# Kernel optimization log

Measured on AMD Instinct MI355X. Metric: run time of the kernel, lower is better.

Reference implementation:

```python
import jax, jax.numpy as jnp
import numpy as np

K_TOP = 10  # module init k


def setup_inputs() -> dict:
    key = jax.random.key(0)
    k1, k2 = jax.random.split(key)
    B, C, H, W = 32, 512, 64, 64
    num_item = 100
    x = jax.random.normal(k1, (B, C, H, W), dtype=jnp.float32)
    # mempool initialized uniform(-stdv, stdv) with stdv = 1/sqrt(dim), as in init_memory
    stdv = 1.0 / np.sqrt(C)
    mempool = jax.random.uniform(k2, (num_item, C), minval=-stdv, maxval=stdv, dtype=jnp.float32)
    return {"x": x, "mempool": mempool}


def reference(x, mempool):
    B, C, H, W = x.shape
    # permute to channels-last, flatten spatial+batch -> queries [N, C]
    q = x.transpose(0, 2, 3, 1).reshape(-1, C)
    # attention over memory items: F.linear(query, mempool) == q @ mempool.T
    att = jax.nn.softmax(q @ mempool.T, axis=1)  # [N, num_item]
    val, idx = jax.lax.top_k(att, K_TOP)          # [N, k]
    val = jax.nn.softmax(val, axis=1)             # renormalize over top-k
    N = q.shape[0]
    # scatter renormalized weights back into a sparse attention matrix
    att_sp = jnp.zeros_like(att).at[jnp.arange(N)[:, None], idx].set(val)
    # reconstruct: F.linear(att, mempool.T) == att @ mempool
    out = (att_sp @ mempool).reshape(B, H, W, C).transpose(0, 3, 1, 2)
    # diversity loss on the memory pool
    m = mempool.shape[0]
    cosim = (mempool @ mempool.T) * 0.5
    off_diag = cosim * (1.0 - jnp.eye(m, dtype=cosim.dtype))
    loss = jnp.mean(jnp.abs(off_diag))
    return (out, loss)
```

## Files before the change

### kernel.cpp

```cpp
#include <hip/hip_runtime.h>
#include <math.h>

#define NITEM 100
#define CDIM 512
#define HW 4096
#define KTOP 10

typedef __attribute__((ext_vector_type(8))) short bf16x8;
typedef __attribute__((ext_vector_type(4))) float f32x4;

__device__ inline unsigned short bf16u(float f) {
  unsigned int u = __float_as_uint(f);
  u += 0x7fffu + ((u >> 16) & 1u);
  return (unsigned short)(u >> 16);
}

__global__ __launch_bounds__(256) __attribute__((amdgpu_waves_per_eu(3, 3)))
void logits_topk(
    const float* __restrict__ x, const float* __restrict__ mp,
    unsigned short* __restrict__ Wd)
{
  __shared__ float qs[2][32 * 128];
  __shared__ float ms[32 * 128];

  const int t   = threadIdx.x;
  const int tc  = t & 15;
  const int trg = t >> 4;
  const int n0  = blockIdx.x * 128;
  const int b   = n0 >> 12;
  const int sp0 = n0 & (HW - 1);
  const float* xb = x + (size_t)b * CDIM * HW + sp0;

  const int w = t >> 6, l = t & 63;
  const int item = t & 127;
  const int half = t >> 7;
  const float* mrow = mp + (size_t)(item < NITEM ? item : 0) * CDIM + 16 * half;

  auto issue_q = [&](int kt, int buf) {
    const int k0 = kt * 32;
    #pragma unroll
    for (int i = 0; i < 4; ++i) {
      const float* src = xb + (size_t)(k0 + 8 * w + 2 * i + (l >> 5)) * HW + (l & 31) * 4;
      float* dst = &qs[buf][(8 * w + 2 * i) * 128];
      __builtin_amdgcn_global_load_lds(
          (const __attribute__((address_space(1))) void*)src,
          (__attribute__((address_space(3))) void*)dst, 16, 0, 0);
    }
  };

  float acc[8][7];
  #pragma unroll
  for (int r = 0; r < 8; ++r)
    #pragma unroll
    for (int j = 0; j < 7; ++j) acc[r][j] = 0.f;

  issue_q(0, 0);
  float4 mv4[4];
  #pragma unroll
  for (int u = 0; u < 4; ++u) mv4[u] = *(const float4*)(mrow + 4 * u);

  int buf = 0;
  #pragma unroll 1
  for (int kt = 0; kt < 16; ++kt) {
    #pragma unroll
    for (int u = 0; u < 4; ++u) {
      ms[(16 * half + 4 * u + 0) * 128 + item] = mv4[u].x;
      ms[(16 * half + 4 * u + 1) * 128 + item] = mv4[u].y;
      ms[(16 * half + 4 * u + 2) * 128 + item] = mv4[u].z;
      ms[(16 * half + 4 * u + 3) * 128 + item] = mv4[u].w;
    }
    __syncthreads();
    if (kt < 15) {
      issue_q(kt + 1, buf ^ 1);
      const int k0n = (kt + 1) * 32;
      #pragma unroll
      for (int u = 0; u < 4; ++u) mv4[u] = *(const float4*)(mrow + k0n + 4 * u);
    }
    const float* qsb = qs[buf];
    #pragma unroll 2
    for (int kk = 0; kk < 32; ++kk) {
      const float* qr = qsb + kk * 128 + 8 * trg;
      const float* mr = ms + kk * 128 + tc;
      float4 qa = *(const float4*)(qr);
      float4 qb = *(const float4*)(qr + 4);
      float mm[7] = {mr[0], mr[16], mr[32], mr[48], mr[64], mr[80], mr[96]};
      float qq[8] = {qa.x, qa.y, qa.z, qa.w, qb.x, qb.y, qb.z, qb.w};
      #pragma unroll
      for (int r = 0; r < 8; ++r)
        #pragma unroll
        for (int j = 0; j < 7; ++j)
          acc[r][j] = __builtin_fmaf(qq[r], mm[j], acc[r][j]);
    }
    __syncthreads();
    buf ^= 1;
  }

  const int baserow = n0 + 8 * trg;
  #pragma unroll
  for (int r = 0; r < 8; ++r) {
    float attv[KTOP]; int id[KTOP];
    float mx = 0.f, Z = 0.f;
    #pragma unroll
    for (int s = 0; s < KTOP; ++s) {
      float bv = -INFINITY; int bi = 0x7fffffff;
      #pragma unroll
      for (int j = 0; j < 7; ++j) {
        bool valid = (j < 6) || (tc < 4);
        float v = valid ? acc[r][j] : -INFINITY;
        if (v > bv) { bv = v; bi = tc + 16 * j; }
      }
      #pragma unroll
      for (int d = 1; d < 16; d <<= 1) {
        float ov = __shfl_xor(bv, d, 16);
        int   oi = __shfl_xor(bi, d, 16);
        if (ov > bv || (ov == bv && oi < bi)) { bv = ov; bi = oi; }
      }
      if (s == 0) {
        mx = bv;
        float zp = 0.f;
        #pragma unroll
        for (int j = 0; j < 7; ++j) {
          bool valid = (j < 6) || (tc < 4);
          zp += valid ? __expf(acc[r][j] - mx) : 0.f;
        }
        #pragma unroll
        for (int d = 1; d < 16; d <<= 1) zp += __shfl_xor(zp, d, 16);
        Z = zp;
      }
      attv[s] = bv; id[s] = bi;
      #pragma unroll
      for (int j = 0; j < 7; ++j)
        if (bi == tc + 16 * j) acc[r][j] = -INFINITY;
    }
    float invZ = 1.f / Z;
    float p0 = invZ;
    float s2 = 0.f, wv[KTOP];
    #pragma unroll
    for (int s = 0; s < KTOP; ++s) {
      float p = __expf(attv[s] - mx) * invZ;
      float e = __expf(p - p0);
      wv[s] = e; s2 += e;
    }
    float inv2 = 1.f / s2;
    unsigned short wb[KTOP];
    #pragma unroll
    for (int s = 0; s < KTOP; ++s) wb[s] = bf16u(wv[s] * inv2);
    unsigned int packed[4];
    #pragma unroll
    for (int q2 = 0; q2 < 4; ++q2) {
      unsigned int lo = 0u, hi = 0u;
      #pragma unroll
      for (int s = 0; s < KTOP; ++s) {
        lo = (id[s] == 8 * tc + 2 * q2)     ? (unsigned int)wb[s] : lo;
        hi = (id[s] == 8 * tc + 2 * q2 + 1) ? (unsigned int)wb[s] : hi;
      }
      packed[q2] = lo | (hi << 16);
    }
    if (tc < 14) {
      uint4 o; o.x = packed[0]; o.y = packed[1]; o.z = packed[2]; o.w = packed[3];
      *(uint4*)(Wd + (size_t)(baserow + r) * 112 + 8 * tc) = o;
    }
  }
}

__global__ __launch_bounds__(256, 2) void recon(
    const float* __restrict__ mp, const unsigned short* __restrict__ Wd,
    float* __restrict__ out)
{
  __shared__ unsigned short Ash[128 * 136];
  __shared__ unsigned short Bsh[128 * 136];
  const int t  = threadIdx.x;
  const int ct = blockIdx.x & 3, nt = blockIdx.x >> 2;
  const int c0 = ct * 128, n0 = nt * 128;
  const int b  = n0 >> 12, sp0 = n0 & (HW - 1);

  #pragma unroll
  for (int j = 0; j < 13; ++j) {
    int task = t + 256 * j;
    if (task < 3200) {
      int k = task >> 5, c4 = (task & 31) << 2;
      float4 v = *(const float4*)(mp + (size_t)k * CDIM + c0 + c4);
      Ash[(c4 + 0) * 136 + k] = bf16u(v.x);
      Ash[(c4 + 1) * 136 + k] = bf16u(v.y);
      Ash[(c4 + 2) * 136 + k] = bf16u(v.z);
      Ash[(c4 + 3) * 136 + k] = bf16u(v.w);
    }
  }
  {
    int c = t >> 1, hf = t & 1;
    unsigned int* A32 = (unsigned int*)Ash;
    #pragma unroll
    for (int j = 0; j < 9; ++j) { int k = 100 + 2 * (hf * 9 + j); A32[(c * 136 + k) >> 1] = 0u; }
  }
  {
    int n = t >> 1, hf = t & 1;
    #pragma unroll
    for (int j = 0; j < 7; ++j) {
      int f = hf * 7 + j;
      *(bf16x8*)(Bsh + n * 136 + 8 * f) = *(const bf16x8*)(Wd + (size_t)(n0 + n) * 112 + 8 * f);
    }
    unsigned int* B32 = (unsigned int*)Bsh;
    #pragma unroll
    for (int j = 0; j < 6; ++j) { int k = 112 + 2 * (hf * 6 + j); B32[(n * 136 + k) >> 1] = 0u; }
  }
  __syncthreads();

  const int w = t >> 6, l = t & 63;
  const int arow = l & 15, kg = l >> 4;
  f32x4 acc[2][8];
  #pragma unroll
  for (int cr = 0; cr < 2; ++cr)
    #pragma unroll
    for (int n = 0; n < 8; ++n) acc[cr][n] = (f32x4){0.f, 0.f, 0.f, 0.f};

  #pragma unroll
  for (int ks = 0; ks < 4; ++ks) {
    bf16x8 a0 = *(bf16x8*)(Ash + ((2 * w + 0) * 16 + arow) * 136 + ks * 32 + kg * 8);
    bf16x8 a1 = *(bf16x8*)(Ash + ((2 * w + 1) * 16 + arow) * 136 + ks * 32 + kg * 8);
    #pragma unroll
    for (int nn = 0; nn < 8; ++nn) {
      bf16x8 bb = *(bf16x8*)(Bsh + (nn * 16 + arow) * 136 + ks * 32 + kg * 8);
      acc[0][nn] = __builtin_amdgcn_mfma_f32_16x16x32_bf16(a0, bb, acc[0][nn], 0, 0, 0);
      acc[1][nn] = __builtin_amdgcn_mfma_f32_16x16x32_bf16(a1, bb, acc[1][nn], 0, 0, 0);
    }
  }

  float* ob = out + (size_t)b * CDIM * HW + sp0;
  #pragma unroll
  for (int cr = 0; cr < 2; ++cr) {
    #pragma unroll
    for (int nn = 0; nn < 8; ++nn) {
      int ncol = nn * 16 + arow;
      #pragma unroll
      for (int j = 0; j < 4; ++j) {
        int cc = c0 + (2 * w + cr) * 16 + kg * 4 + j;
        ob[(size_t)cc * HW + ncol] = acc[cr][nn][j];
      }
    }
  }
}

__global__ void loss_partial(const float* __restrict__ mp, float* __restrict__ part)
{
  __shared__ float mi[CDIM];
  __shared__ float red[4];
  const int i = blockIdx.x;
  const int t = threadIdx.x;
  for (int k = t; k < CDIM; k += 256) mi[k] = mp[i * CDIM + k];
  __syncthreads();
  float v = 0.f;
  if (t < NITEM && t != i) {
    const float* mj = mp + t * CDIM;
    float d = 0.f;
    #pragma unroll 8
    for (int k = 0; k < CDIM; ++k) d += mi[k] * mj[k];
    v = fabsf(0.5f * d);
  }
  #pragma unroll
  for (int o = 32; o > 0; o >>= 1) v += __shfl_down(v, o, 64);
  if ((t & 63) == 0) red[t >> 6] = v;
  __syncthreads();
  if (t == 0) part[i] = red[0] + red[1] + red[2] + red[3];
}

__global__ void loss_final(const float* __restrict__ part, float* __restrict__ out_loss)
{
  if (threadIdx.x == 0) {
    float s = 0.f;
    for (int i = 0; i < NITEM; ++i) s += part[i];
    *out_loss = s / (float)(NITEM * NITEM);
  }
}

extern "C" void kernel_launch(void* const* d_in, const int* in_sizes, int n_in,
                              void* d_out, int out_size, void* d_ws, size_t ws_size,
                              hipStream_t stream) {
  const float* x  = (const float*)d_in[0];
  const float* mp = (const float*)d_in[1];
  float* out = (float*)d_out;
  unsigned short* Wd = (unsigned short*)d_ws;
  float* part = (float*)((char*)d_ws + (size_t)131072 * 112 * 2);

  logits_topk<<<1024, 256, 0, stream>>>(x, mp, Wd);
  recon<<<4096, 256, 0, stream>>>(mp, Wd, out);
  loss_partial<<<NITEM, 256, 0, stream>>>(mp, part);
  loss_final<<<1, 64, 0, stream>>>(part, out + (out_size - 1));
}
```

Baseline: 374.2 us.

## Read pre-transposed mempool straight from global and drop its LDS staging

A small pre-kernel writes a zero-padded, transposed copy of the memory pool (K x 128). It uses the tail of the output buffer as scratch, and the recon kernel overwrites that region later. The logits kernel now loads the memory-pool operand with float4 global loads that should hit in cache, instead of staging it through LDS. Each thread gets a contiguous 8x8 register tile. The k-tile is halved to 16 and one barrier per iteration is removed. The aim is to cut LDS stores, LDS reads and barrier cost. In exchange the kernel has global-load latency in the inner loop, an extra launch, and 128 computed items instead of 112.

```diff
diff --git a/kernel.cpp b/kernel.cpp
--- a/kernel.cpp
+++ b/kernel.cpp
@@ -15,13 +15,18 @@
   return (unsigned short)(u >> 16);
 }
 
+__global__ void make_mpT(const float* __restrict__ mp, float* __restrict__ mpT) {
+  int idx = blockIdx.x * 256 + threadIdx.x;
+  int k = idx >> 7, item = idx & 127;
+  mpT[idx] = (item < NITEM) ? mp[item * CDIM + k] : 0.f;
+}
+
 __global__ __launch_bounds__(256) __attribute__((amdgpu_waves_per_eu(3, 3)))
 void logits_topk(
-    const float* __restrict__ x, const float* __restrict__ mp,
+    const float* __restrict__ x, const float* __restrict__ mpT,
     unsigned short* __restrict__ Wd)
 {
-  __shared__ float qs[2][32 * 128];
-  __shared__ float ms[32 * 128];
+  __shared__ float qs[2][16 * 128];
 
   const int t   = threadIdx.x;
   const int tc  = t & 15;
@@ -30,68 +35,53 @@
   const int b   = n0 >> 12;
   const int sp0 = n0 & (HW - 1);
   const float* xb = x + (size_t)b * CDIM * HW + sp0;
-
   const int w = t >> 6, l = t & 63;
-  const int item = t & 127;
-  const int half = t >> 7;
-  const float* mrow = mp + (size_t)(item < NITEM ? item : 0) * CDIM + 16 * half;
 
   auto issue_q = [&](int kt, int buf) {
-    const int k0 = kt * 32;
-    #pragma unroll
-    for (int i = 0; i < 4; ++i) {
-      const float* src = xb + (size_t)(k0 + 8 * w + 2 * i + (l >> 5)) * HW + (l & 31) * 4;
-      float* dst = &qs[buf][(8 * w + 2 * i) * 128];
+    const int k0 = kt * 16;
+    #pragma unroll
+    for (int i = 0; i < 2; ++i) {
+      const int slot0 = w * 64 + 256 * i;
+      const int kk = (slot0 >> 5) + (l >> 5);
+      const float* src = xb + (size_t)(k0 + kk) * HW + 4 * (l & 31);
+      float* dst = &qs[buf][slot0 * 4];
       __builtin_amdgcn_global_load_lds(
           (const __attribute__((address_space(1))) void*)src,
           (__attribute__((address_space(3))) void*)dst, 16, 0, 0);
     }
   };
 
-  float acc[8][7];
+  float acc[8][8];
   #pragma unroll
   for (int r = 0; r < 8; ++r)
     #pragma unroll
-    for (int j = 0; j < 7; ++j) acc[r][j] = 0.f;
+    for (int j = 0; j < 8; ++j) acc[r][j] = 0.f;
 
   issue_q(0, 0);
-  float4 mv4[4];
-  #pragma unroll
-  for (int u = 0; u < 4; ++u) mv4[u] = *(const float4*)(mrow + 4 * u);
 
   int buf = 0;
   #pragma unroll 1
-  for (int kt = 0; kt < 16; ++kt) {
-    #pragma unroll
-    for (int u = 0; u < 4; ++u) {
-      ms[(16 * half + 4 * u + 0) * 128 + item] = mv4[u].x;
-      ms[(16 * half + 4 * u + 1) * 128 + item] = mv4[u].y;
-      ms[(16 * half + 4 * u + 2) * 128 + item] = mv4[u].z;
-      ms[(16 * half + 4 * u + 3) * 128 + item] = mv4[u].w;
-    }
+  for (int kt = 0; kt < 32; ++kt) {
     __syncthreads();
-    if (kt < 15) {
-      issue_q(kt + 1, buf ^ 1);
-      const int k0n = (kt + 1) * 32;
-      #pragma unroll
-      for (int u = 0; u < 4; ++u) mv4[u] = *(const float4*)(mrow + k0n + 4 * u);
-    }
+    if (kt < 31) issue_q(kt + 1, buf ^ 1);
+    const int k0 = kt * 16;
     const float* qsb = qs[buf];
-    #pragma unroll 2
-    for (int kk = 0; kk < 32; ++kk) {
+    #pragma unroll 4
+    for (int kk = 0; kk < 16; ++kk) {
       const float* qr = qsb + kk * 128 + 8 * trg;
-      const float* mr = ms + kk * 128 + tc;
+      const float* mr = mpT + (size_t)(k0 + kk) * 128 + 8 * tc;
       float4 qa = *(const float4*)(qr);
-      float4 qb = *(const float4*)(qr + 4);
-      float mm[7] = {mr[0], mr[16], mr[32], mr[48], mr[64], mr[80], mr[96]};
-      float qq[8] = {qa.x, qa.y, qa.z, qa.w, qb.x, qb.y, qb.z, qb.w};
+      float4 qb4 = *(const float4*)(qr + 4);
+      float4 ma = *(const float4*)(mr);
+      float4 mb = *(const float4*)(mr + 4);
+      float qq[8] = {qa.x, qa.y, qa.z, qa.w, qb4.x, qb4.y, qb4.z, qb4.w};
+      float mm[8] = {ma.x, ma.y, ma.z, ma.w, mb.x, mb.y, mb.z, mb.w};
       #pragma unroll
       for (int r = 0; r < 8; ++r)
         #pragma unroll
-        for (int j = 0; j < 7; ++j)
+        for (int j = 0; j < 8; ++j)
           acc[r][j] = __builtin_fmaf(qq[r], mm[j], acc[r][j]);
     }
-    __syncthreads();
     buf ^= 1;
   }
 
@@ -104,10 +94,10 @@
     for (int s = 0; s < KTOP; ++s) {
       float bv = -INFINITY; int bi = 0x7fffffff;
       #pragma unroll
-      for (int j = 0; j < 7; ++j) {
-        bool valid = (j < 6) || (tc < 4);
-        float v = valid ? acc[r][j] : -INFINITY;
-        if (v > bv) { bv = v; bi = tc + 16 * j; }
+      for (int jj = 0; jj < 8; ++jj) {
+        bool valid = (8 * tc + jj) < NITEM;
+        float v = valid ? acc[r][jj] : -INFINITY;
+        if (v > bv) { bv = v; bi = 8 * tc + jj; }
       }
       #pragma unroll
       for (int d = 1; d < 16; d <<= 1) {
@@ -119,9 +109,9 @@
         mx = bv;
         float zp = 0.f;
         #pragma unroll
-        for (int j = 0; j < 7; ++j) {
-          bool valid = (j < 6) || (tc < 4);
-          zp += valid ? __expf(acc[r][j] - mx) : 0.f;
+        for (int jj = 0; jj < 8; ++jj) {
+          bool valid = (8 * tc + jj) < NITEM;
+          zp += valid ? __expf(acc[r][jj] - mx) : 0.f;
         }
         #pragma unroll
         for (int d = 1; d < 16; d <<= 1) zp += __shfl_xor(zp, d, 16);
@@ -129,8 +119,8 @@
       }
       attv[s] = bv; id[s] = bi;
       #pragma unroll
-      for (int j = 0; j < 7; ++j)
-        if (bi == tc + 16 * j) acc[r][j] = -INFINITY;
+      for (int jj = 0; jj < 8; ++jj)
+        if (bi == 8 * tc + jj) acc[r][jj] = -INFINITY;
     }
     float invZ = 1.f / Z;
     float p0 = invZ;
@@ -281,7 +271,10 @@
   unsigned short* Wd = (unsigned short*)d_ws;
   float* part = (float*)((char*)d_ws + (size_t)131072 * 112 * 2);
 
-  logits_topk<<<1024, 256, 0, stream>>>(x, mp, Wd);
+  float* mpT = out + (size_t)60 * 1024 * 1024;
+
+  make_mpT<<<256, 256, 0, stream>>>(mp, mpT);
+  logits_topk<<<1024, 256, 0, stream>>>(x, mpT, Wd);
   recon<<<4096, 256, 0, stream>>>(mp, Wd, out);
   loss_partial<<<NITEM, 256, 0, stream>>>(mp, part);
   loss_final<<<1, 64, 0, stream>>>(part, out + (out_size - 1));
```

After: 1.092 ms. +191.9%, slower.
